# Kernel optimization log

Measured on AMD Instinct MI355X. Metric: run time of the kernel, lower is better.

## Reference

```python
import jax, jax.numpy as jnp
import numpy as np

H = 16  # hidden_size
D = 32  # input_size == output_size
B = 2048
T = 512


def _leaky(x):
    return jnp.where(x >= 0, x, 0.01 * x)  # nn.LeakyReLU default slope


def _lstm_cell(x, h, c, Wih, Whh, bih, bhh):
    # torch.nn.LSTMCell gate order: i, f, g, o
    g = x @ Wih.T + h @ Whh.T + bih + bhh  # [B, 4H]
    i, f, gg, o = jnp.split(g, 4, axis=-1)
    i = jax.nn.sigmoid(i)
    f = jax.nn.sigmoid(f)
    gg = jnp.tanh(gg)
    o = jax.nn.sigmoid(o)
    c = f * c + i * gg
    h = o * jnp.tanh(c)
    return h, c


def setup_inputs() -> dict:
    key = jax.random.key(0)
    ks = jax.random.split(key, 20)
    s = 1.0 / np.sqrt(H)
    u = lambda k, shape: jax.random.uniform(k, shape, jnp.float32, -s, s)
    return {
        "seq": jax.random.normal(ks[0], (B, T, D), jnp.float32),
        "pre_w1": u(ks[1], (H, D)), "pre_b1": u(ks[2], (H,)),
        "pre_w2": u(ks[3], (H, H)), "pre_b2": u(ks[4], (H,)),
        "pre_w3": u(ks[5], (H, H)), "pre_b3": u(ks[6], (H,)),
        "enc_Wih": u(ks[7], (4 * H, H)), "enc_Whh": u(ks[8], (4 * H, H)),
        "enc_bih": u(ks[9], (4 * H,)), "enc_bhh": u(ks[10], (4 * H,)),
        "h2l_w1": u(ks[11], (H, H)), "h2l_b1": u(ks[12], (H,)),
        "h2l_w2": u(ks[13], (H, H)), "h2l_b2": u(ks[14], (H,)),
        "post_w": u(ks[15], (D, H)), "post_b": u(ks[16], (D,)),
    }


def reference(seq, pre_w1, pre_b1, pre_w2, pre_b2, pre_w3, pre_b3,
              enc_Wih, enc_Whh, enc_bih, enc_bhh,
              h2l_w1, h2l_b1, h2l_w2, h2l_b2, post_w, post_b):
    Bx = seq.shape[0]
    # pre MLP: Linear -> LeakyReLU -> Linear -> LeakyReLU -> Linear
    x = _leaky(seq @ pre_w1.T + pre_b1)
    x = _leaky(x @ pre_w2.T + pre_b2)
    x = x @ pre_w3.T + pre_b3  # [B, T, H]

    start0 = x[:, -1, :]
    h0 = jnp.zeros((Bx, H), seq.dtype)
    c0 = jnp.zeros((Bx, H), seq.dtype)

    # encoder loop over time (serial)
    def enc_step(carry, xt):
        h, c = carry
        h, c = _lstm_cell(xt, h, c, enc_Wih, enc_Whh, enc_bih, enc_bhh)
        return (h, c), None

    (h, c), _ = jax.lax.scan(enc_step, (h0, c0), jnp.swapaxes(x, 0, 1))

    # decoder loop (note: source reuses self.encoder cell here)
    def dec_step(carry, _):
        h, c, start = carry
        h, c = _lstm_cell(start, h, c, enc_Wih, enc_Whh, enc_bih, enc_bhh)
        start = _leaky(h @ h2l_w1.T + h2l_b1) @ h2l_w2.T + h2l_b2
        out = h @ post_w.T + post_b  # [B, D]
        return (h, c, start), out

    _, outs = jax.lax.scan(dec_step, (h, c, start0), None, length=seq.shape[1])
    # outputs[:, -1 - i] = out_i  ->  reverse time, then [B, T, D]
    outputs = jnp.swapaxes(outs[::-1], 0, 1)
    return (outputs, outputs)
```

## Files before the change

### kernel.cpp

```cpp
#include <hip/hip_runtime.h>

typedef unsigned int u32;
typedef float v2f __attribute__((ext_vector_type(2)));

#define T_LEN 512
#define BATCH 2048
#define OSTRIDE ((size_t)BATCH * T_LEN * 32)

__device__ __forceinline__ float rlf(float v, int l) {
  return __int_as_float(__builtin_amdgcn_readlane(__float_as_int(v), l));
}
#define QB(v, pat) __int_as_float(__builtin_amdgcn_mov_dpp(__float_as_int(v), (pat), 0xF, 0xF, false))

__global__ __launch_bounds__(256) void prenet_kernel(
    const float* __restrict__ seq,
    const float* __restrict__ w1, const float* __restrict__ b1,
    const float* __restrict__ w2, const float* __restrict__ b2,
    const float* __restrict__ w3, const float* __restrict__ b3,
    float* __restrict__ xws) {
  __shared__ float sW[1072];
  const int tid = threadIdx.x;
  sW[tid] = w1[tid];
  sW[256 + tid] = w1[256 + tid];
  sW[528 + tid] = w2[tid];
  sW[800 + tid] = w3[tid];
  if (tid < 16) {
    sW[512 + tid] = b1[tid];
    sW[784 + tid] = b2[tid];
    sW[1056 + tid] = b3[tid];
  }
  __syncthreads();

  const size_t r = (size_t)blockIdx.x * 256 + tid;
  const float* sp = seq + r * 32;

  float in[32];
#pragma unroll
  for (int q = 0; q < 8; ++q) {
    float4 v = ((const float4*)sp)[q];
    in[q * 4 + 0] = v.x;
    in[q * 4 + 1] = v.y;
    in[q * 4 + 2] = v.z;
    in[q * 4 + 3] = v.w;
  }

  const float4* wv = (const float4*)sW;

  float y1[16];
#pragma unroll
  for (int j = 0; j < 16; ++j) {
    float a0 = 0.f, a1 = 0.f, a2 = 0.f, a3 = 0.f;
#pragma unroll
    for (int q = 0; q < 8; ++q) {
      float4 w = wv[j * 8 + q];
      a0 = __builtin_fmaf(w.x, in[q * 4 + 0], a0);
      a1 = __builtin_fmaf(w.y, in[q * 4 + 1], a1);
      a2 = __builtin_fmaf(w.z, in[q * 4 + 2], a2);
      a3 = __builtin_fmaf(w.w, in[q * 4 + 3], a3);
    }
    float s = (a0 + a1) + (a2 + a3) + sW[512 + j];
    y1[j] = s >= 0.f ? s : 0.01f * s;
  }

  float y2[16];
#pragma unroll
  for (int j = 0; j < 16; ++j) {
    float a0 = 0.f, a1 = 0.f, a2 = 0.f, a3 = 0.f;
#pragma unroll
    for (int q = 0; q < 4; ++q) {
      float4 w = wv[132 + j * 4 + q];
      a0 = __builtin_fmaf(w.x, y1[q * 4 + 0], a0);
      a1 = __builtin_fmaf(w.y, y1[q * 4 + 1], a1);
      a2 = __builtin_fmaf(w.z, y1[q * 4 + 2], a2);
      a3 = __builtin_fmaf(w.w, y1[q * 4 + 3], a3);
    }
    float s = (a0 + a1) + (a2 + a3) + sW[784 + j];
    y2[j] = s >= 0.f ? s : 0.01f * s;
  }

  float y3[16];
#pragma unroll
  for (int j = 0; j < 16; ++j) {
    float a0 = 0.f, a1 = 0.f, a2 = 0.f, a3 = 0.f;
#pragma unroll
    for (int q = 0; q < 4; ++q) {
      float4 w = wv[200 + j * 4 + q];
      a0 = __builtin_fmaf(w.x, y2[q * 4 + 0], a0);
      a1 = __builtin_fmaf(w.y, y2[q * 4 + 1], a1);
      a2 = __builtin_fmaf(w.z, y2[q * 4 + 2], a2);
      a3 = __builtin_fmaf(w.w, y2[q * 4 + 3], a3);
    }
    y3[j] = (a0 + a1) + (a2 + a3) + sW[1056 + j];
  }

  float* op = xws + r * 16;
#pragma unroll
  for (int q = 0; q < 4; ++q)
    ((float4*)op)[q] =
        make_float4(y3[q * 4 + 0], y3[q * 4 + 1], y3[q * 4 + 2], y3[q * 4 + 3]);
}

#define CELL(XP)                                                            \
  do {                                                                      \
    v2f A = {bias, 0.f}, Bv = {0.f, 0.f};                                   \
    _Pragma("unroll") for (int j = 0; j < 8; j += 2) {                      \
      A = __builtin_elementwise_fma(wih2[j], XP[j], A);                     \
      Bv = __builtin_elementwise_fma(wih2[j + 1], XP[j + 1], Bv);           \
    }                                                                       \
    _Pragma("unroll") for (int j = 0; j < 8; j += 2) {                      \
      A = __builtin_elementwise_fma(whh2[j], HU[j], A);                     \
      Bv = __builtin_elementwise_fma(whh2[j + 1], HU[j + 1], Bv);           \
    }                                                                       \
    A = A + Bv;                                                             \
    float g = A.x + A.y;       \
    float ee = __expf(g);                                                   \
    float rr = __builtin_amdgcn_rcpf(1.0f + ee);                            \
    float act = __builtin_fmaf(sa, rr, sb);                                 \
    float ii = QB(act, 0x00);                                               \
    float ff = QB(act, 0x55);                                               \
    float gg = QB(act, 0xAA);                                               \
    float oo = QB(act, 0xFF);                                               \
    c = __builtin_fmaf(ff, c, ii * gg);                                     \
    float te = __expf(c + c);                                               \
    float th = __builtin_fmaf(                                              \
        -2.0f, __builtin_amdgcn_rcpf(1.0f + te), 1.0f);                     \
    h = oo * th;                                                            \
    _Pragma("unroll") for (int j = 0; j < 8; ++j) {                         \
      HU[j].x = rlf(h, 8 * j);                                              \
      HU[j].y = rlf(h, 8 * j + 4);                                          \
    }                                                                       \
  } while (0)

__global__ __launch_bounds__(256) void lstm_rec_kernel(
    const float* __restrict__ Wih, const float* __restrict__ Whh,
    const float* __restrict__ bih, const float* __restrict__ bhh,
    const float* __restrict__ hw1, const float* __restrict__ hb1,
    const float* __restrict__ hw2, const float* __restrict__ hb2,
    const float* __restrict__ pw, const float* __restrict__ pb,
    const float* __restrict__ xws, float* __restrict__ out) {
  const int lane = threadIdx.x & 63;
  const int bu =
      __builtin_amdgcn_readfirstlane(blockIdx.x * 4 + (threadIdx.x >> 6));
  const int hr = lane >> 2;
  const int gi = (lane & 3) * 16 + hr;
  const bool isT = (lane & 3) == 2;

  const float sK = isT ? 2.0f : -1.0f;
  const float sa = isT ? -2.0f : 1.0f;
  const float sb = isT ? 1.0f : 0.0f;

  v2f wih2[8], whh2[8];
#pragma unroll
  for (int j = 0; j < 8; ++j) {
    wih2[j].x = Wih[gi * 16 + 2 * j] * sK;
    wih2[j].y = Wih[gi * 16 + 2 * j + 1] * sK;
    whh2[j].x = Whh[gi * 16 + 2 * j] * sK;
    whh2[j].y = Whh[gi * 16 + 2 * j + 1] * sK;
  }
  const float bias = (bih[gi] + bhh[gi]) * sK;

  float h = 0.f, c = 0.f;
  v2f HU[8];
#pragma unroll
  for (int j = 0; j < 8; ++j) HU[j] = (v2f){0.f, 0.f};

  const float* xb = xws + (size_t)bu * (T_LEN * 16);

  v2f xs0[8], xs1[8];
#pragma unroll
  for (int j = 0; j < 8; ++j) {
    xs0[j].x = xb[2 * j];
    xs0[j].y = xb[2 * j + 1];
  }
  for (int t = 0; t < T_LEN; t += 2) {
    const float* n1 = xb + (size_t)(t + 1) * 16;
#pragma unroll
    for (int j = 0; j < 8; ++j) {
      xs1[j].x = n1[2 * j];
      xs1[j].y = n1[2 * j + 1];
    }
    CELL(xs0);
    const int t2 = (t + 2 < T_LEN) ? (t + 2) : (T_LEN - 1);
    const float* n2 = xb + (size_t)t2 * 16;
#pragma unroll
    for (int j = 0; j < 8; ++j) {
      xs0[j].x = n2[2 * j];
      xs0[j].y = n2[2 * j + 1];
    }
    CELL(xs1);
  }

  v2f mr2[8], w22[8];
  const int mrow = (lane < 32) ? lane : (lane & 15);
  const float* msrc = (lane < 32) ? (pw + mrow * 16) : (hw1 + mrow * 16);
  const float mbias = (lane < 32) ? pb[mrow] : hb1[mrow];
  const float sl = (lane < 32) ? 1.0f : 0.01f;
  const int w2row = lane & 15;
#pragma unroll
  for (int j = 0; j < 8; ++j) {
    mr2[j].x = msrc[2 * j];
    mr2[j].y = msrc[2 * j + 1];
    w22[j].x = hw2[w2row * 16 + 2 * j];
    w22[j].y = hw2[w2row * 16 + 2 * j + 1];
  }
  const float b2r = hb2[w2row];

  v2f XK[8];
  {
    const float* src = xb + (size_t)(T_LEN - 1) * 16;
#pragma unroll
    for (int j = 0; j < 8; ++j) {
      XK[j].x = src[2 * j];
      XK[j].y = src[2 * j + 1];
    }
  }

  const size_t obase = (size_t)bu * (T_LEN * 32) + (lane & 31);

  for (int t = 0; t < T_LEN; ++t) {
    CELL(XK);

    v2f A = {mbias, 0.f}, Bv = {0.f, 0.f};
#pragma unroll
    for (int j = 0; j < 8; j += 2) {
      A = __builtin_elementwise_fma(mr2[j], HU[j], A);
      Bv = __builtin_elementwise_fma(mr2[j + 1], HU[j + 1], Bv);
    }
    A = A + Bv;
    float y0 = A.x + A.y;
    float yv = fmaxf(y0, y0 * sl);

    v2f TU[8];
#pragma unroll
    for (int j = 0; j < 8; ++j) {
      TU[j].x = rlf(yv, 32 + 2 * j);
      TU[j].y = rlf(yv, 33 + 2 * j);
    }

    v2f C2 = {b2r, 0.f}, D2 = {0.f, 0.f};
#pragma unroll
    for (int j = 0; j < 8; j += 2) {
      C2 = __builtin_elementwise_fma(w22[j], TU[j], C2);
      D2 = __builtin_elementwise_fma(w22[j + 1], TU[j + 1], D2);
    }
    C2 = C2 + D2;
    float sv = C2.x + C2.y;

#pragma unroll
    for (int j = 0; j < 8; ++j) {
      XK[j].x = rlf(sv, 2 * j);
      XK[j].y = rlf(sv, 2 * j + 1);
    }

    if (lane < 32) {
      const size_t off = obase + (size_t)(T_LEN - 1 - t) * 32;
      out[off] = yv;
      out[off + OSTRIDE] = yv;
    }
  }
}

extern "C" void kernel_launch(void* const* d_in, const int* in_sizes, int n_in,
                              void* d_out, int out_size, void* d_ws, size_t ws_size,
                              hipStream_t stream) {
  const float* seq = (const float*)d_in[0];
  const float* pre_w1 = (const float*)d_in[1];
  const float* pre_b1 = (const float*)d_in[2];
  const float* pre_w2 = (const float*)d_in[3];
  const float* pre_b2 = (const float*)d_in[4];
  const float* pre_w3 = (const float*)d_in[5];
  const float* pre_b3 = (const float*)d_in[6];
  const float* enc_Wih = (const float*)d_in[7];
  const float* enc_Whh = (const float*)d_in[8];
  const float* enc_bih = (const float*)d_in[9];
  const float* enc_bhh = (const float*)d_in[10];
  const float* h2l_w1 = (const float*)d_in[11];
  const float* h2l_b1 = (const float*)d_in[12];
  const float* h2l_w2 = (const float*)d_in[13];
  const float* h2l_b2 = (const float*)d_in[14];
  const float* post_w = (const float*)d_in[15];
  const float* post_b = (const float*)d_in[16];

  float* xws = (float*)d_ws;

  prenet_kernel<<<dim3(4096), dim3(256), 0, stream>>>(
      seq, pre_w1, pre_b1, pre_w2, pre_b2, pre_w3, pre_b3, xws);

  lstm_rec_kernel<<<dim3(512), dim3(256), 0, stream>>>(
      enc_Wih, enc_Whh, enc_bih, enc_bhh, h2l_w1, h2l_b1, h2l_w2, h2l_b2,
      post_w, post_b, xws, (float*)d_out);
}
```

Measured before the change: 757.6 us.

## Fold h2l second linear into decoder input weights, drop shared-memory prenet weights

Precomputes Wih·W2 and the combined bias so the decoder feeds the LeakyReLU hidden layer straight into the LSTM cell. This removes one 16x16 matvec, a readlane broadcast round and a reduction from each serial decoder step. It also replaces packed v2f FMAs with scalar FMAs and reads prenet weights from global or constant memory instead of staging them in LDS. The folded weights change the rounding order, and scalar FMAs may issue more instructions than the packed form.

```diff
diff --git a/kernel.cpp b/kernel.cpp
--- a/kernel.cpp
+++ b/kernel.cpp
@@ -1,11 +1,7 @@
 #include <hip/hip_runtime.h>
 
-typedef unsigned int u32;
-typedef float v2f __attribute__((ext_vector_type(2)));
-
 #define T_LEN 512
-#define BATCH 2048
-#define OSTRIDE ((size_t)BATCH * T_LEN * 32)
+#define OSTRIDE ((size_t)2048 * 512 * 32)
 
 __device__ __forceinline__ float rlf(float v, int l) {
   return __int_as_float(__builtin_amdgcn_readlane(__float_as_int(v), l));
@@ -18,19 +14,7 @@
     const float* __restrict__ w2, const float* __restrict__ b2,
     const float* __restrict__ w3, const float* __restrict__ b3,
     float* __restrict__ xws) {
-  __shared__ float sW[1072];
   const int tid = threadIdx.x;
-  sW[tid] = w1[tid];
-  sW[256 + tid] = w1[256 + tid];
-  sW[528 + tid] = w2[tid];
-  sW[800 + tid] = w3[tid];
-  if (tid < 16) {
-    sW[512 + tid] = b1[tid];
-    sW[784 + tid] = b2[tid];
-    sW[1056 + tid] = b3[tid];
-  }
-  __syncthreads();
-
   const size_t r = (size_t)blockIdx.x * 256 + tid;
   const float* sp = seq + r * 32;
 
@@ -44,53 +28,48 @@
     in[q * 4 + 3] = v.w;
   }
 
-  const float4* wv = (const float4*)sW;
-
   float y1[16];
 #pragma unroll
   for (int j = 0; j < 16; ++j) {
-    float a0 = 0.f, a1 = 0.f, a2 = 0.f, a3 = 0.f;
-#pragma unroll
-    for (int q = 0; q < 8; ++q) {
-      float4 w = wv[j * 8 + q];
-      a0 = __builtin_fmaf(w.x, in[q * 4 + 0], a0);
-      a1 = __builtin_fmaf(w.y, in[q * 4 + 1], a1);
-      a2 = __builtin_fmaf(w.z, in[q * 4 + 2], a2);
-      a3 = __builtin_fmaf(w.w, in[q * 4 + 3], a3);
-    }
-    float s = (a0 + a1) + (a2 + a3) + sW[512 + j];
+    float a0 = b1[j], a1 = 0.f, a2 = 0.f, a3 = 0.f;
+#pragma unroll
+    for (int k = 0; k < 32; k += 4) {
+      a0 = __builtin_fmaf(w1[j * 32 + k + 0], in[k + 0], a0);
+      a1 = __builtin_fmaf(w1[j * 32 + k + 1], in[k + 1], a1);
+      a2 = __builtin_fmaf(w1[j * 32 + k + 2], in[k + 2], a2);
+      a3 = __builtin_fmaf(w1[j * 32 + k + 3], in[k + 3], a3);
+    }
+    float s = (a0 + a1) + (a2 + a3);
     y1[j] = s >= 0.f ? s : 0.01f * s;
   }
 
   float y2[16];
 #pragma unroll
   for (int j = 0; j < 16; ++j) {
-    float a0 = 0.f, a1 = 0.f, a2 = 0.f, a3 = 0.f;
-#pragma unroll
-    for (int q = 0; q < 4; ++q) {
-      float4 w = wv[132 + j * 4 + q];
-      a0 = __builtin_fmaf(w.x, y1[q * 4 + 0], a0);
-      a1 = __builtin_fmaf(w.y, y1[q * 4 + 1], a1);
-      a2 = __builtin_fmaf(w.z, y1[q * 4 + 2], a2);
-      a3 = __builtin_fmaf(w.w, y1[q * 4 + 3], a3);
-    }
-    float s = (a0 + a1) + (a2 + a3) + sW[784 + j];
+    float a0 = b2[j], a1 = 0.f, a2 = 0.f, a3 = 0.f;
+#pragma unroll
+    for (int k = 0; k < 16; k += 4) {
+      a0 = __builtin_fmaf(w2[j * 16 + k + 0], y1[k + 0], a0);
+      a1 = __builtin_fmaf(w2[j * 16 + k + 1], y1[k + 1], a1);
+      a2 = __builtin_fmaf(w2[j * 16 + k + 2], y1[k + 2], a2);
+      a3 = __builtin_fmaf(w2[j * 16 + k + 3], y1[k + 3], a3);
+    }
+    float s = (a0 + a1) + (a2 + a3);
     y2[j] = s >= 0.f ? s : 0.01f * s;
   }
 
   float y3[16];
 #pragma unroll
   for (int j = 0; j < 16; ++j) {
-    float a0 = 0.f, a1 = 0.f, a2 = 0.f, a3 = 0.f;
-#pragma unroll
-    for (int q = 0; q < 4; ++q) {
-      float4 w = wv[200 + j * 4 + q];
-      a0 = __builtin_fmaf(w.x, y2[q * 4 + 0], a0);
-      a1 = __builtin_fmaf(w.y, y2[q * 4 + 1], a1);
-      a2 = __builtin_fmaf(w.z, y2[q * 4 + 2], a2);
-      a3 = __builtin_fmaf(w.w, y2[q * 4 + 3], a3);
-    }
-    y3[j] = (a0 + a1) + (a2 + a3) + sW[1056 + j];
+    float a0 = b3[j], a1 = 0.f, a2 = 0.f, a3 = 0.f;
+#pragma unroll
+    for (int k = 0; k < 16; k += 4) {
+      a0 = __builtin_fmaf(w3[j * 16 + k + 0], y2[k + 0], a0);
+      a1 = __builtin_fmaf(w3[j * 16 + k + 1], y2[k + 1], a1);
+      a2 = __builtin_fmaf(w3[j * 16 + k + 2], y2[k + 2], a2);
+      a3 = __builtin_fmaf(w3[j * 16 + k + 3], y2[k + 3], a3);
+    }
+    y3[j] = (a0 + a1) + (a2 + a3);
   }
 
   float* op = xws + r * 16;
@@ -100,19 +79,22 @@
         make_float4(y3[q * 4 + 0], y3[q * 4 + 1], y3[q * 4 + 2], y3[q * 4 + 3]);
 }
 
-#define CELL(XP)                                                            \
+#define CELL(WX, XA, BB)                                                    \
   do {                                                                      \
-    v2f A = {bias, 0.f}, Bv = {0.f, 0.f};                                   \
-    _Pragma("unroll") for (int j = 0; j < 8; j += 2) {                      \
-      A = __builtin_elementwise_fma(wih2[j], XP[j], A);                     \
-      Bv = __builtin_elementwise_fma(wih2[j + 1], XP[j + 1], Bv);           \
+    float a0 = (BB), a1 = 0.f, a2 = 0.f, a3 = 0.f;                          \
+    _Pragma("unroll") for (int k = 0; k < 16; k += 4) {                     \
+      a0 = __builtin_fmaf(WX[k + 0], XA[k + 0], a0);                        \
+      a1 = __builtin_fmaf(WX[k + 1], XA[k + 1], a1);                        \
+      a2 = __builtin_fmaf(WX[k + 2], XA[k + 2], a2);                        \
+      a3 = __builtin_fmaf(WX[k + 3], XA[k + 3], a3);                        \
     }                                                                       \
-    _Pragma("unroll") for (int j = 0; j < 8; j += 2) {                      \
-      A = __builtin_elementwise_fma(whh2[j], HU[j], A);                     \
-      Bv = __builtin_elementwise_fma(whh2[j + 1], HU[j + 1], Bv);           \
+    _Pragma("unroll") for (int k = 0; k < 16; k += 4) {                     \
+      a0 = __builtin_fmaf(whhr[k + 0], hk[k + 0], a0);                      \
+      a1 = __builtin_fmaf(whhr[k + 1], hk[k + 1], a1);                      \
+      a2 = __builtin_fmaf(whhr[k + 2], hk[k + 2], a2);                      \
+      a3 = __builtin_fmaf(whhr[k + 3], hk[k + 3], a3);                      \
     }                                                                       \
-    A = A + Bv;                                                             \
-    float g = A.x + A.y;       \
+    float g = (a0 + a1) + (a2 + a3);                                        \
     float ee = __expf(g);                                                   \
     float rr = __builtin_amdgcn_rcpf(1.0f + ee);                            \
     float act = __builtin_fmaf(sa, rr, sb);                                 \
@@ -121,14 +103,10 @@
     float gg = QB(act, 0xAA);                                               \
     float oo = QB(act, 0xFF);                                               \
     c = __builtin_fmaf(ff, c, ii * gg);                                     \
-    float te = __expf(c + c);                                               \
     float th = __builtin_fmaf(                                              \
-        -2.0f, __builtin_amdgcn_rcpf(1.0f + te), 1.0f);                     \
+        -2.0f, __builtin_amdgcn_rcpf(1.0f + __expf(c + c)), 1.0f);          \
     h = oo * th;                                                            \
-    _Pragma("unroll") for (int j = 0; j < 8; ++j) {                         \
-      HU[j].x = rlf(h, 8 * j);                                              \
-      HU[j].y = rlf(h, 8 * j + 4);                                          \
-    }                                                                       \
+    _Pragma("unroll") for (int k = 0; k < 16; ++k) hk[k] = rlf(h, 4 * k);   \
   } while (0)
 
 __global__ __launch_bounds__(256) void lstm_rec_kernel(
@@ -149,113 +127,92 @@
   const float sa = isT ? -2.0f : 1.0f;
   const float sb = isT ? 1.0f : 0.0f;
 
-  v2f wih2[8], whh2[8];
-#pragma unroll
-  for (int j = 0; j < 8; ++j) {
-    wih2[j].x = Wih[gi * 16 + 2 * j] * sK;
-    wih2[j].y = Wih[gi * 16 + 2 * j + 1] * sK;
-    whh2[j].x = Whh[gi * 16 + 2 * j] * sK;
-    whh2[j].y = Whh[gi * 16 + 2 * j + 1] * sK;
+  float wihr[16], whhr[16];
+#pragma unroll
+  for (int k = 0; k < 16; ++k) {
+    wihr[k] = Wih[gi * 16 + k] * sK;
+    whhr[k] = Whh[gi * 16 + k] * sK;
   }
   const float bias = (bih[gi] + bhh[gi]) * sK;
 
   float h = 0.f, c = 0.f;
-  v2f HU[8];
-#pragma unroll
-  for (int j = 0; j < 8; ++j) HU[j] = (v2f){0.f, 0.f};
+  float hk[16];
+#pragma unroll
+  for (int k = 0; k < 16; ++k) hk[k] = 0.f;
 
   const float* xb = xws + (size_t)bu * (T_LEN * 16);
 
-  v2f xs0[8], xs1[8];
-#pragma unroll
-  for (int j = 0; j < 8; ++j) {
-    xs0[j].x = xb[2 * j];
-    xs0[j].y = xb[2 * j + 1];
-  }
+  float xA[16], xB[16];
+#pragma unroll
+  for (int k = 0; k < 16; ++k) xA[k] = xb[k];
   for (int t = 0; t < T_LEN; t += 2) {
     const float* n1 = xb + (size_t)(t + 1) * 16;
 #pragma unroll
-    for (int j = 0; j < 8; ++j) {
-      xs1[j].x = n1[2 * j];
-      xs1[j].y = n1[2 * j + 1];
-    }
-    CELL(xs0);
+    for (int k = 0; k < 16; ++k) xB[k] = n1[k];
+    CELL(wihr, xA, bias);
     const int t2 = (t + 2 < T_LEN) ? (t + 2) : (T_LEN - 1);
     const float* n2 = xb + (size_t)t2 * 16;
 #pragma unroll
-    for (int j = 0; j < 8; ++j) {
-      xs0[j].x = n2[2 * j];
-      xs0[j].y = n2[2 * j + 1];
-    }
-    CELL(xs1);
-  }
-
-  v2f mr2[8], w22[8];
+    for (int k = 0; k < 16; ++k) xA[k] = n2[k];
+    CELL(wihr, xB, bias);
+  }
+
   const int mrow = (lane < 32) ? lane : (lane & 15);
   const float* msrc = (lane < 32) ? (pw + mrow * 16) : (hw1 + mrow * 16);
   const float mbias = (lane < 32) ? pb[mrow] : hb1[mrow];
   const float sl = (lane < 32) ? 1.0f : 0.01f;
-  const int w2row = lane & 15;
-#pragma unroll
-  for (int j = 0; j < 8; ++j) {
-    mr2[j].x = msrc[2 * j];
-    mr2[j].y = msrc[2 * j + 1];
-    w22[j].x = hw2[w2row * 16 + 2 * j];
-    w22[j].y = hw2[w2row * 16 + 2 * j + 1];
-  }
-  const float b2r = hb2[w2row];
-
-  v2f XK[8];
+  float mr[16];
+#pragma unroll
+  for (int k = 0; k < 16; ++k) mr[k] = msrc[k];
+
+  float Mr[16];
+#pragma unroll
+  for (int k = 0; k < 16; ++k) Mr[k] = 0.f;
+#pragma unroll
+  for (int j = 0; j < 16; ++j) {
+#pragma unroll
+    for (int k = 0; k < 16; ++k)
+      Mr[k] = __builtin_fmaf(wihr[j], hw2[j * 16 + k], Mr[k]);
+  }
+  float mbias2 = bias;
+#pragma unroll
+  for (int j = 0; j < 16; ++j)
+    mbias2 = __builtin_fmaf(wihr[j], hb2[j], mbias2);
+
+  float xk[16];
   {
     const float* src = xb + (size_t)(T_LEN - 1) * 16;
 #pragma unroll
-    for (int j = 0; j < 8; ++j) {
-      XK[j].x = src[2 * j];
-      XK[j].y = src[2 * j + 1];
-    }
-  }
-
+    for (int k = 0; k < 16; ++k) xk[k] = src[k];
+  }
+
+  float uk[16];
   const size_t obase = (size_t)bu * (T_LEN * 32) + (lane & 31);
 
+  CELL(wihr, xk, bias);
+
   for (int t = 0; t < T_LEN; ++t) {
-    CELL(XK);
-
-    v2f A = {mbias, 0.f}, Bv = {0.f, 0.f};
-#pragma unroll
-    for (int j = 0; j < 8; j += 2) {
-      A = __builtin_elementwise_fma(mr2[j], HU[j], A);
-      Bv = __builtin_elementwise_fma(mr2[j + 1], HU[j + 1], Bv);
-    }
-    A = A + Bv;
-    float y0 = A.x + A.y;
+    float p0 = mbias, p1 = 0.f, p2 = 0.f, p3 = 0.f;
+#pragma unroll
+    for (int k = 0; k < 16; k += 4) {
+      p0 = __builtin_fmaf(mr[k + 0], hk[k + 0], p0);
+      p1 = __builtin_fmaf(mr[k + 1], hk[k + 1], p1);
+      p2 = __builtin_fmaf(mr[k + 2], hk[k + 2], p2);
+      p3 = __builtin_fmaf(mr[k + 3], hk[k + 3], p3);
+    }
+    float y0 = (p0 + p1) + (p2 + p3);
     float yv = fmaxf(y0, y0 * sl);
-
-    v2f TU[8];
-#pragma unroll
-    for (int j = 0; j < 8; ++j) {
-      TU[j].x = rlf(yv, 32 + 2 * j);
-      TU[j].y = rlf(yv, 33 + 2 * j);
-    }
-
-    v2f C2 = {b2r, 0.f}, D2 = {0.f, 0.f};
-#pragma unroll
-    for (int j = 0; j < 8; j += 2) {
-      C2 = __builtin_elementwise_fma(w22[j], TU[j], C2);
-      D2 = __builtin_elementwise_fma(w22[j + 1], TU[j + 1], D2);
-    }
-    C2 = C2 + D2;
-    float sv = C2.x + C2.y;
-
-#pragma unroll
-    for (int j = 0; j < 8; ++j) {
-      XK[j].x = rlf(sv, 2 * j);
-      XK[j].y = rlf(sv, 2 * j + 1);
-    }
 
     if (lane < 32) {
       const size_t off = obase + (size_t)(T_LEN - 1 - t) * 32;
       out[off] = yv;
       out[off + OSTRIDE] = yv;
+    }
+
+    if (t + 1 < T_LEN) {
+#pragma unroll
+      for (int k = 0; k < 16; ++k) uk[k] = rlf(yv, 32 + k);
+      CELL(Mr, uk, mbias2);
     }
   }
 }
```

Result: slower. 783.0 us (+3.4%).
